# Optimization experiments

Hardware: AMD Instinct MI355X
Metric: run time of the kernel (lower is better)

The kernel has to match this reference:

```python
import jax, jax.numpy as jnp
import numpy as np

MAX_LR = 0.01  # max_learning_rate
NS_A, NS_B, NS_C = 3.4445, -4.7750, 2.0315  # muon Newton-Schulz quintic coefficients


def newtonschulz5(G, steps=5, eps=1e-7):
    # Orthogonalize the last two dims of G (batched over leading dims).
    transpose = G.shape[-2] > G.shape[-1]
    X = jnp.swapaxes(G, -2, -1) if transpose else G
    X = X / (jnp.linalg.norm(X, axis=(-2, -1), keepdims=True) + eps)
    for _ in range(steps):
        A = X @ jnp.swapaxes(X, -2, -1)
        Bm = NS_B * A + NS_C * (A @ A)
        X = NS_A * X + Bm @ X
    return jnp.swapaxes(X, -2, -1) if transpose else X


def setup_inputs() -> dict:
    key = jax.random.key(0)
    ks = jax.random.split(key, 9)
    B, N, D, H, DH = 4, 1024, 1024, 8, 64
    s = D ** -0.5  # scale fast-weight init for numerical sanity (math unchanged)
    return {
        'tokens': jax.random.normal(ks[0], (B, N, D), jnp.float32),
        'wq': jax.random.normal(ks[1], (H, D, DH), jnp.float32) * s,
        'wk': jax.random.normal(ks[2], (H, D, DH), jnp.float32) * s,
        'wv': jax.random.normal(ks[3], (H, D, DH), jnp.float32) * s,
        'wo': jax.random.normal(ks[4], (H, DH, D), jnp.float32) * s,
        'w_lr': jax.random.normal(ks[5], (D, 2), jnp.float32) * 0.02,      # to_learning_rate (no bias)
        'w_target': jax.random.normal(ks[6], (D, D), jnp.float32) * 0.02,  # to_target_values linear (no bias)
        'w_gates': jax.random.normal(ks[7], (D, H), jnp.float32) * 0.02,   # to_gates linear (no bias)
        'rms_w': jnp.ones((D,), jnp.float32),                              # RMSNorm weight
    }


def reference(tokens, wq, wk, wv, wo, w_lr, w_target, w_gates, rms_w):
    N = tokens.shape[1]
    scale = wq.shape[-1] ** -0.5
    eps = jnp.finfo(tokens.dtype).eps

    # RMSNorm
    t = tokens * jax.lax.rsqrt(jnp.mean(tokens * tokens, -1, keepdims=True) + eps) * rms_w

    # gates: b n h -> b h n 1
    gates = jnp.swapaxes(jax.nn.sigmoid(t @ w_gates), -2, -1)[..., None]

    # per-batch fast weights == shared params (past_mem=None), broadcast over b via einsum
    q = jnp.einsum('bnd,hde->bhne', t, wq)
    k = jnp.einsum('bnd,hde->bhne', t, wk)
    v = jnp.einsum('bnd,hde->bhne', t, wv)

    score = jnp.einsum('bhie,bhje->bhij', q, k) * scale
    causal_mask = jnp.triu(jnp.ones((N, N), bool), 1)
    score = jnp.where(causal_mask, -jnp.finfo(score.dtype).max, score)
    attn = jax.nn.softmax(score, axis=-1)
    out = jnp.einsum('bhij,bhje->bhie', attn, v) * gates
    pred_values = jnp.einsum('bhne,hed->bnd', out, wo)

    # target values: linear + LayerNorm (no affine) on shifted tokens
    tv = t[:, 1:] @ w_target
    tv = (tv - tv.mean(-1, keepdims=True)) * jax.lax.rsqrt(tv.var(-1, keepdims=True) + 1e-5)

    # drop last position everywhere
    ts = t[:, :-1]
    pv = pred_values[:, :-1]
    o = out[:, :, :-1]
    g = gates[:, :, :-1]
    a = attn[:, :, :-1, :-1]
    qs, ks_, vs = q[:, :, :-1], k[:, :, :-1], v[:, :, :-1]

    lrs = jax.nn.sigmoid(ts @ w_lr) * MAX_LR  # b (n-1) 2
    lr, mlr = lrs[..., 0], lrs[..., 1]

    # hand-derived backward through the attention fast-weight readout
    error = tv - pv
    dout = jnp.einsum('bnd,hed->bhne', error, wo)
    du = dout * g
    delta = jnp.sum(dout * o, -1, keepdims=True)
    dv = jnp.einsum('bhij,bhie->bhje', a, du)
    dattn = jnp.einsum('bhje,bhie->bhij', vs, du)
    dscore = scale * a * (dattn - delta)
    dq = jnp.einsum('bhje,bhij->bhie', ks_, dscore)
    dk = jnp.einsum('bhie,bhij->bhje', qs, dscore)

    t_qk = ts * lr[..., None]
    t_v = ts * mlr[..., None]
    o_wo = o * mlr[:, None, :, None]

    dwq = jnp.einsum('bhie,bid->bhde', dq, t_qk)
    dwk = jnp.einsum('bhje,bjd->bhde', dk, t_qk)
    dwv = jnp.einsum('bhje,bjd->bhde', dv, t_v)
    dwo = jnp.einsum('bnd,bhne->bhed', error, o_wo)

    dwv = newtonschulz5(dwv)  # muon orthogonalization
    dwo = newtonschulz5(dwo)

    return pred_values, dwq, dwk, dwv, dwo
```

## Files before the change

kernel.cpp:

```cpp
#include <hip/hip_runtime.h>
#include <hip/hip_bf16.h>
#include <math.h>

#define BB 4
#define NN 1024
#define DD 1024
#define HH 8
#define DH 64
#define NSR 1023

#define NS_Ac 3.4445f
#define NS_Bc (-4.775f)
#define NS_Cc 2.0315f

typedef short bf16x8 __attribute__((ext_vector_type(8)));
typedef float f32x4 __attribute__((ext_vector_type(4)));
#define MFMA16(a,b,c) __builtin_amdgcn_mfma_f32_16x16x32_bf16(a,b,c,0,0,0)

#define QS 72
#define TS 40
#define GS 40

static __device__ __forceinline__ float ldin(const void* p, size_t i, int f) {
  return f ? ((const float*)p)[i] : __bfloat162float(((const __hip_bfloat16*)p)[i]);
// ... 74 lines not shown
  const void* src; short* dst; int sld, dld, srow0, scol0, drow0; size_t soff = 0;
  if (bx < 384) {
    int x = bx & 15, y = bx >> 4;
    int n0 = y*64; int which = n0 >> 9, h = (n0 >> 6) & 7;
    src = (which==0) ? wq : (which==1) ? wk : wv;
    soff = (size_t)h*65536;
    sld = 64; dld = 1024; srow0 = x*64; scol0 = 0; drow0 = n0; dst = BqkvT;
  } else if (bx < 640) {
    int r = bx - 384; int x = r & 15, y = r >> 4;
    src = w_target; dst = wtT; sld = 1024; dld = 1024;
    srow0 = x*64; scol0 = y*64; drow0 = scol0;
  } else {
    int r = bx - 640; int x = r & 7, y = r >> 3;
    src = wo; dst = woT2; sld = 1024; dld = 512;
    srow0 = x*64; scol0 = y*64; drow0 = scol0;
  }
  __shared__ float T[64][65];
  int r4 = tid >> 4, c4 = (tid & 15)*4;
  for (int rr = r4; rr < 64; rr += 16)
#pragma unroll
    for (int j = 0; j < 4; j++)
      T[rr][c4+j] = ldin(src, soff + (size_t)(srow0+rr)*sld + scol0 + c4 + j, f);
  __syncthreads();
  int dc = tid >> 2, seg = tid & 3;
  bf16x8 o1, o2;
#pragma unroll
  for (int j = 0; j < 8; j++) { o1[j] = f2bs(T[seg*16+j][dc]); o2[j] = f2bs(T[seg*16+8+j][dc]); }
  *(bf16x8*)&dst[(size_t)(drow0+dc)*dld + srow0 + seg*16]     = o1;
  *(bf16x8*)&dst[(size_t)(drow0+dc)*dld + srow0 + seg*16 + 8] = o2;
}

__global__ __launch_bounds__(256) void k_transp(
    const float* __restrict__ src, size_t sStepZ, int sld,
    short* __restrict__ dst, size_t dStepZ, int dld,
    const float* __restrict__ coef, int zIsBh, int nz)
{
  int z = blockIdx.z;
  const float* sb = src + (size_t)z*sStepZ;
  short* db = dst + (size_t)z*dStepZ;
  const float* cb = coef ? coef + (size_t)(zIsBh ? (z>>3) : z)*1024 : (const float*)0;
  int x0 = blockIdx.x*64, y0 = blockIdx.y*64;
  __shared__ float T[64][65];
  int tid = threadIdx.x;
  int r4 = tid >> 4, c4 = (tid & 15)*4;
  for (int rr = r4; rr < 64; rr += 16) {
    int rg = x0 + rr;
    bool val = rg < nz;
    float cf = val ? (cb ? cb[rg] : 1.f) : 0.f;
    float4 v = val ? *(const float4*)&sb[(size_t)rg*sld + y0 + c4] : make_float4(0,0,0,0);
    T[rr][c4+0] = v.x*cf; T[rr][c4+1] = v.y*cf; T[rr][c4+2] = v.z*cf; T[rr][c4+3] = v.w*cf;
  }
  __syncthreads();
  int dc = tid >> 2, seg = tid & 3;
  bf16x8 o1, o2;
#pragma unroll
  for (int j = 0; j < 8; j++) { o1[j] = f2bs(T[seg*16+j][dc]); o2[j] = f2bs(T[seg*16+8+j][dc]); }
  *(bf16x8*)&db[(size_t)(y0+dc)*dld + x0 + seg*16]     = o1;
  *(bf16x8*)&db[(size_t)(y0+dc)*dld + x0 + seg*16 + 8] = o2;
}

__global__ __launch_bounds__(256) void k_transp5(
    const float* __restrict__ dq, const float* __restrict__ dk, const float* __restrict__ dv,
    const float* __restrict__ predf, const float* __restrict__ o,
    short* __restrict__ dqT, short* __restrict__ dkT, short* __restrict__ dvT,
    short* __restrict__ errT, short* __restrict__ oT,
    const float* __restrict__ lr, const float* __restrict__ mlr)
{
  int bx = blockIdx.x;
  const float* src; short* dst; const float* cb; int sld, dld, x0, y0;
  size_t sStep, dStep; int z;
  if (bx < 1536) {
    int which = bx >> 9; int r = bx & 511;
    z = r >> 4; x0 = (r & 15)*64; y0 = 0;
    sld = 64; dld = 1024; sStep = 65536; dStep = 65536;
    if (which == 0)      { src = dq; dst = dqT; cb = lr; }
    else if (which == 1) { src = dk; dst = dkT; cb = lr; }
    else                 { src = dv; dst = dvT; cb = mlr; }
    cb += (size_t)(z >> 3)*1024;
  } else if (bx < 2560) {
    int r = bx - 1536; z = r >> 8; x0 = (r & 15)*64; y0 = ((r >> 4) & 15)*64;
    src = predf; dst = errT; cb = (const float*)0;
    sld = 1024; dld = 1024; sStep = 1048576; dStep = 1048576;
  } else {
    int r = bx - 2560; z = r >> 7; x0 = (r & 15)*64; y0 = ((r >> 4) & 7)*64;
    src = o; dst = oT; cb = mlr + (size_t)z*1024;
    sld = 512; dld = 1024; sStep = 524288; dStep = 524288;
  }
  src += (size_t)z*sStep; dst += (size_t)z*dStep;
  __shared__ float T[64][65];
  int tid = threadIdx.x;
  int r4 = tid >> 4, c4 = (tid & 15)*4;
  for (int rr = r4; rr < 64; rr += 16) {
    int rg = x0 + rr;
    bool val = rg < 1023;
    float cf = val ? (cb ? cb[rg] : 1.f) : 0.f;
    float4 v = val ? *(const float4*)&src[(size_t)rg*sld + y0 + c4] : make_float4(0,0,0,0);
    T[rr][c4+0] = v.x*cf; T[rr][c4+1] = v.y*cf; T[rr][c4+2] = v.z*cf; T[rr][c4+3] = v.w*cf;
  }
  __syncthreads();
  int dc = tid >> 2, seg = tid & 3;
  bf16x8 o1, o2;
#pragma unroll
  for (int j = 0; j < 8; j++) { o1[j] = f2bs(T[seg*16+j][dc]); o2[j] = f2bs(T[seg*16+8+j][dc]); }
  *(bf16x8*)&dst[(size_t)(y0+dc)*dld + x0 + seg*16]     = o1;
  *(bf16x8*)&dst[(size_t)(y0+dc)*dld + x0 + seg*16 + 8] = o2;
}

__global__ void k_rmsnorm(const void* __restrict__ tokens, const float* __restrict__ rms_f,
                          const float* __restrict__ gw, const float* __restrict__ lrw,
                          float* __restrict__ t, short* __restrict__ t_bf,
                          float* __restrict__ gates, float* __restrict__ lr, float* __restrict__ mlr,
                          const int* __restrict__ flag) {
  const int f = *flag;
  int row = blockIdx.x;
  int b = row >> 10, n = row & 1023;
  __shared__ float red[256];
  __shared__ float red2[4][10];
  float xv[4]; float acc = 0.f;
#pragma unroll
  for (int i = 0; i < 4; i++) {
    xv[i] = ldin(tokens, (size_t)row*DD + threadIdx.x + 256*i, f);
    acc += xv[i]*xv[i];
  }
  red[threadIdx.x] = acc; __syncthreads();
  for (int s = 128; s > 0; s >>= 1) { if (threadIdx.x < s) red[threadIdx.x] += red[threadIdx.x+s]; __syncthreads(); }
  float r = rsqrtf(red[0] / DD + 1.1920929e-07f);
  float a10[10] = {0,0,0,0,0,0,0,0,0,0};
#pragma unroll
  for (int i = 0; i < 4; i++) {
    int d = threadIdx.x + 256*i;
    float v = xv[i] * r * rms_f[d];
    t[(size_t)row*DD + d] = v;
    t_bf[(size_t)row*DD + d] = f2bs(v);
#pragma unroll
    for (int h = 0; h < HH; h++) a10[h] += v * gw[d*HH + h];
    a10[8] += v * lrw[d*2];
    a10[9] += v * lrw[d*2+1];
  }
  int lane = threadIdx.x & 63, w = threadIdx.x >> 6;
#pragma unroll
  for (int c = 0; c < 10; c++) {
    float a = a10[c];
    for (int s = 32; s > 0; s >>= 1) a += __shfl_xor(a, s, 64);
    if (lane == 0) red2[w][c] = a;
  }
  __syncthreads();
  if (threadIdx.x < 10) {
    int c = threadIdx.x;
    float sum = red2[0][c]+red2[1][c]+red2[2][c]+red2[3][c];
    float sg = 1.f / (1.f + __expf(-sum));
    if (c < 8)      gates[((size_t)b*HH + c)*NN + n] = sg;
    else if (c == 8) lr[row]  = sg * 0.01f;
    else             mlr[row] = sg * 0.01f;
  }
}

__global__ __launch_bounds__(256) void k_gemm_bf(
    const short* __restrict__ A, const short* __restrict__ B,
    int lda, int ldb, int K, int M, int rowmode, int ep,
    size_t aStepBh, size_t aStepB, size_t bStepBh, size_t bStepB,
    float* __restrict__ O0, short* __restrict__ OS, void* __restrict__ OD,
    size_t out_off, const float* __restrict__ gates, const int* __restrict__ flag,
    const short* __restrict__ A2, const short* __restrict__ B2,
    size_t bStepB2, size_t out_off2, int ldb2)
{
  int z = blockIdx.z;
  const short* Au = A; const short* Bu = B;
  size_t bStepBv = bStepB; size_t out_offv = out_off;
  int epv = ep; int ldbv = ldb;
  if (ep == 4 && z >= 32) { Bu = B2; out_offv = out_off2; z -= 32; }
  if (ep == 5 && z >= 32) { Au = A2; Bu = B2; bStepBv = bStepB2; ldbv = ldb2; epv = 6; z -= 32; }
  int zb = z >> 3;
  const short* Ab = Au + (size_t)z*aStepBh + (size_t)zb*aStepB;
  const short* Bb = Bu + (size_t)z*bStepBh + (size_t)zb*bStepBv;
  int m0 = blockIdx.x*64, n0 = blockIdx.y*64;
  __shared__ __align__(16) short AsBs[5120];
  short* As = AsBs;
  short* Bs = AsBs + 2560;
  int tid = threadIdx.x;
  int lane = tid & 63, w = tid >> 6;
  int l15 = lane & 15, quad = lane >> 4;
  int row = tid >> 2, col8 = (tid & 3)*8;
  int r = m0 + row;
  int arow;
  if (rowmode == 1)      { int b = r / 1023; arow = r + b + 1; }
  else if (rowmode == 2) { int b = r / 1023; arow = r + b; }
  else arow = r;
  bool aval = (r < M);
  const short* Ap = Ab + (size_t)arow*lda + col8;
  const short* Bp = Bb + (size_t)(n0+row)*ldbv + col8;
  f32x4 acc[4] = {fz4(),fz4(),fz4(),fz4()};
  bf16x8 av = aval ? *(const bf16x8*)(Ap) : bz8();
  bf16x8 bv = *(const bf16x8*)(Bp);
  for (int kb = 0; kb < K; kb += 32) {
    __syncthreads();
    *(bf16x8*)&As[row*GS + col8] = av;
    *(bf16x8*)&Bs[row*GS + col8] = bv;
    __syncthreads();
    if (kb + 32 < K) {
      av = aval ? *(const bf16x8*)(Ap + kb + 32) : bz8();
      bv = *(const bf16x8*)(Bp + kb + 32);
    }
    bf16x8 afr = *(const bf16x8*)&As[(w*16 + l15)*GS + quad*8];
#pragma unroll
    for (int es = 0; es < 4; es++) {
      bf16x8 bfr = *(const bf16x8*)&Bs[(es*16 + l15)*GS + quad*8];
      acc[es] = MFMA16(afr, bfr, acc[es]);
    }
  }
  const int f = flag ? *flag : 1;
#pragma unroll
  for (int es = 0; es < 4; es++) {
#pragma unroll
    for (int rix = 0; rix < 4; rix++) {
      int rr = m0 + w*16 + quad*4 + rix;
      if (rr >= M) continue;
      int c = n0 + es*16 + l15;
      float val = acc[es][rix];
      if (epv == 0) {
        int which = c >> 9; int h = (c >> 6) & 7; int e = c & 63;
        int b = rr >> 10; int n = rr & 1023;
        OS[(size_t)which*2097152 + (((size_t)b*8 + h)*1024 + n)*64 + e] = f2bs(val);
      } else if (epv == 1) {
        O0[(size_t)rr*1024 + c] = val;
        stout(OD, (size_t)rr*1024 + c, val, f);
      } else if (epv == 2) {
        O0[(size_t)rr*1024 + c] = val;
      } else if (epv == 3) {
        int b = rr / 1023; int n = rr % 1023;
        int h = c >> 6;
        float g = gates[((size_t)b*8 + h)*1024 + n];
        OS[((size_t)b*1024 + n)*512 + c] = f2bs(val * g);
      } else if (epv == 4) {
        stout(OD, out_offv + ((size_t)z*1024 + rr)*64 + c, val, f);
      } else if (epv == 5) {
        O0[((size_t)z*64 + rr)*1024 + c] = val;
      } else {
        O0[((size_t)(32 + z)*64 + rr)*1024 + c] = val;
      }
    }
  }
  if (epv == 0 && (n0 >> 9) == 2) {
    short* vt = (short*)OD;
    int h = (n0 >> 6) & 7;
    int bb = m0 >> 10;
    int bh = bb*8 + h;
    int nloc = m0 & 1023;
    __syncthreads();
#pragma unroll
    for (int es = 0; es < 4; es++)
#pragma unroll
      for (int rix = 0; rix < 4; rix++)
        AsBs[(es*16 + l15)*72 + (w*16 + quad*4 + rix)] = f2bs(acc[es][rix]);
    __syncthreads();
    int e = tid >> 2, nseg = (tid & 3)*16;
    bf16x8 v1 = *(const bf16x8*)&AsBs[e*72 + nseg];
    bf16x8 v2 = *(const bf16x8*)&AsBs[e*72 + nseg + 8];
    size_t dsti = ((size_t)bh*64 + e)*1024 + nloc + nseg;
    *(bf16x8*)&vt[dsti]     = v1;
    *(bf16x8*)&vt[dsti + 8] = v2;
  }
}

__global__ __launch_bounds__(256) void k_attn_fwd(
    const short* __restrict__ qb, const short* __restrict__ kb, const short* __restrict__ vbT,
    const float* __restrict__ gates,
    float* __restrict__ o, short* __restrict__ o_bf,
    float* __restrict__ mrow, float* __restrict__ lrow)
{
  int pp = blockIdx.x >> 8;
  int xx = (blockIdx.x >> 5) & 7;
  int bh = blockIdx.x & 31;
  int it = pp ? xx : (15 - xx);
  int i0 = it*64;
  int b = bh >> 3, h = bh & 7;
  __shared__ __align__(16) short Qs[64*QS];
  __shared__ __align__(16) short Ks[32*QS];
  __shared__ __align__(16) short VsT[64*TS];
  __shared__ __align__(16) short Ps[64*TS];
  int tid = threadIdx.x;
  int lane = tid & 63, w = tid >> 6;
  int l15 = lane & 15, quad = lane >> 4;
  int sr = tid >> 3, sc = (tid & 7) * 8;
  int sr2 = tid >> 2, sc2 = (tid & 3) * 8;
  int rsw = (l15 >> 2) & 3;
  for (int rr = sr; rr < 64; rr += 32)
    *(bf16x8*)&Qs[rr*QS + sc] = *(const bf16x8*)&qb[((size_t)bh*1024 + i0 + rr)*64 + sc];
  f32x4 oa[4] = {fz4(),fz4(),fz4(),fz4()};
  float m_st[4] = {-1e30f,-1e30f,-1e30f,-1e30f};
  float l_st[4] = {0.f,0.f,0.f,0.f};
  int jiters = 2*it + 2;
  bf16x8 rk = *(const bf16x8*)&kb[((size_t)bh*1024 + sr)*64 + sc];
  bf16x8 rv = *(const bf16x8*)&vbT[((size_t)bh*64 + sr2)*1024 + sc2];
  for (int jc = 0; jc < jiters; jc++) {
    int j0 = jc*32;
    __syncthreads();
    *(bf16x8*)&Ks[sr*QS + sc]    = rk;
    *(bf16x8*)&VsT[sr2*TS + sc2] = rv;
    __syncthreads();
    if (jc + 1 < jiters) {
      int j1 = j0 + 32;
      rk = *(const bf16x8*)&kb[((size_t)bh*1024 + j1 + sr)*64 + sc];
      rv = *(const bf16x8*)&vbT[((size_t)bh*64 + sr2)*1024 + j1 + sc2];
    }
    f32x4 sa[2] = {fz4(),fz4()};
#pragma unroll
    for (int kc = 0; kc < 64; kc += 32) {
      bf16x8 afr = *(const bf16x8*)&Qs[(w*16 + l15)*QS + kc + quad*8];
#pragma unroll
      for (int ni = 0; ni < 2; ni++) {
        bf16x8 bfr = *(const bf16x8*)&Ks[(ni*16 + l15)*QS + kc + quad*8];
        sa[ni] = MFMA16(afr, bfr, sa[ni]);
      }
    }
#pragma unroll
    for (int r = 0; r < 4; r++) {
      int gi = i0 + w*16 + quad*4 + r;
      float s0 = sa[0][r]*0.125f, s1 = sa[1][r]*0.125f;
      if (j0 + l15 > gi)      s0 = -1e30f;
      if (j0 + 16 + l15 > gi) s1 = -1e30f;
      float rm = fmaxf(s0, s1);
      rm = fmaxf(rm, __shfl_xor(rm, 1, 64));
      rm = fmaxf(rm, __shfl_xor(rm, 2, 64));
      rm = fmaxf(rm, __shfl_xor(rm, 4, 64));
      rm = fmaxf(rm, __shfl_xor(rm, 8, 64));
      float m_new = fmaxf(m_st[r], rm);
      float alpha = __expf(m_st[r] - m_new);
      float p0 = __expf(s0 - m_new), p1 = __expf(s1 - m_new);
      float rs = p0 + p1;
      rs += __shfl_xor(rs, 1, 64);
      rs += __shfl_xor(rs, 2, 64);
      rs += __shfl_xor(rs, 4, 64);
      rs += __shfl_xor(rs, 8, 64);
      l_st[r] = l_st[r]*alpha + rs;
      m_st[r] = m_new;
#pragma unroll
      for (int es = 0; es < 4; es++) oa[es][r] *= alpha;
      int rowp = w*16 + quad*4 + r;
      int lo3 = l15 & 7, g0 = l15 >> 3;
      Ps[rowp*TS + ((( g0      ^ quad) << 3) | lo3)] = f2bs(p0);
      Ps[rowp*TS + ((((g0 | 2) ^ quad) << 3) | lo3)] = f2bs(p1);
    }
    bf16x8 pa = *(const bf16x8*)&Ps[(w*16 + l15)*TS + ((quad ^ rsw) << 3)];
#pragma unroll
    for (int es = 0; es < 4; es++) {
      bf16x8 bv = *(const bf16x8*)&VsT[(es*16 + l15)*TS + quad*8];
      oa[es] = MFMA16(pa, bv, oa[es]);
    }
  }
#pragma unroll
  for (int r = 0; r < 4; r++) {
    int gi = i0 + w*16 + quad*4 + r;
    float g = gates[(size_t)bh*1024 + gi] / l_st[r];
#pragma unroll
    for (int es = 0; es < 4; es++) {
      float val = oa[es][r] * g;
      size_t oi = ((size_t)b*1024 + gi)*512 + h*64 + es*16 + l15;
      o[oi] = val;
      o_bf[oi] = f2bs(val);
    }
    if (l15 == 0) {
      mrow[(size_t)bh*1024 + gi] = m_st[r];
      lrow[(size_t)bh*1024 + gi] = l_st[r];
    }
  }
}

__global__ void k_lnsub(const float* __restrict__ tvbuf, float* __restrict__ predf,
                        short* __restrict__ err_bf) {
  int r = blockIdx.x; int b = r / 1023; int prow = r + b;
  const float* tvr = tvbuf + (size_t)r*1024;
  __shared__ float red[256];
  float s1 = 0.f, s2 = 0.f;
  float xv[4];
#pragma unroll
  for (int i = 0; i < 4; i++) {
    xv[i] = tvr[threadIdx.x + 256*i];
    s1 += xv[i]; s2 += xv[i]*xv[i];
  }
  red[threadIdx.x] = s1; __syncthreads();
  for (int s = 128; s > 0; s >>= 1){ if (threadIdx.x < s) red[threadIdx.x] += red[threadIdx.x+s]; __syncthreads(); }
  float mean = red[0] / 1024.f; __syncthreads();
  red[threadIdx.x] = s2; __syncthreads();
  for (int s = 128; s > 0; s >>= 1){ if (threadIdx.x < s) red[threadIdx.x] += red[threadIdx.x+s]; __syncthreads(); }
  float var = red[0]/1024.f - mean*mean;
  float rstd = rsqrtf(var + 1e-5f);
  float* er = predf + (size_t)prow*1024;
#pragma unroll
  for (int i = 0; i < 4; i++) {
    int d = threadIdx.x + 256*i;
    float e = (xv[i]-mean)*rstd - er[d];
    er[d] = e;
    err_bf[(size_t)prow*1024 + d] = f2bs(e);
  }
}

__global__ __launch_bounds__(256) void k_t16(const short* __restrict__ qv, const short* __restrict__ du,
                                             short* __restrict__ kbT, short* __restrict__ duT,
                                             short* __restrict__ qbT,
                                             const float* __restrict__ o, const float* __restrict__ gates,
                                             float* __restrict__ delta) {
  int bx = blockIdx.x; int tid = threadIdx.x;
  if (bx >= 1536) {
    int r = bx - 1536; int b = r / 1023; int n = r % 1023;
    int w = tid >> 6, lane = tid & 63;
    size_t base = ((size_t)b*1024 + n)*512;
    float p1 = bs2f(du[base + tid])       * o[base + tid];
    float p2 = bs2f(du[base + tid + 256]) * o[base + tid + 256];
    for (int s = 32; s > 0; s >>= 1) { p1 += __shfl_xor(p1, s, 64); p2 += __shfl_xor(p2, s, 64); }
    if (lane == 0) {
      size_t i1 = ((size_t)b*8 + w)*1024 + n;
      size_t i2 = ((size_t)b*8 + w + 4)*1024 + n;
      delta[i1] = p1 / gates[i1];
// ... 102 lines not shown
        rdu  = (g1 < NSR) ? *(const bf16x8*)&du_bf[((size_t)b*1024 + g1)*512 + h*64 + sc] : bz8();
        rqT  = *(const bf16x8*)&qbT[((size_t)bh*64 + sr2)*1024 + i1 + sc2];
        rduT = *(const bf16x8*)&duT[((size_t)bh*64 + sr2)*1024 + i1 + sc2];
        if (tid < 32) {
          int gi2 = i1 + tid;
          rm = mrow[(size_t)bh*1024 + gi2];
          rl = lrow[(size_t)bh*1024 + gi2];
          rd = (gi2 < NSR) ? delta[(size_t)bh*1024 + gi2] : 0.f;
        }
      }
      f32x4 st[2] = {fz4(),fz4()};
      f32x4 dt[2] = {fz4(),fz4()};
#pragma unroll
      for (int kc = 0; kc < 64; kc += 32) {
        bf16x8 ak = *(const bf16x8*)&Ks[(w*16 + l15)*QS + kc + quad*8];
        bf16x8 av = *(const bf16x8*)&Vs[(w*16 + l15)*QS + kc + quad*8];
#pragma unroll
        for (int ni = 0; ni < 2; ni++) {
          bf16x8 bq = *(const bf16x8*)&Qs[(ni*16 + l15)*QS + kc + quad*8];
          bf16x8 bd = *(const bf16x8*)&DUs[(ni*16 + l15)*QS + kc + quad*8];
          st[ni] = MFMA16(ak, bq, st[ni]);
          dt[ni] = MFMA16(av, bd, dt[ni]);
        }
      }
#pragma unroll
      for (int ni = 0; ni < 2; ni++)
#pragma unroll
        for (int r = 0; r < 4; r++) {
          int gj = j0 + w*16 + quad*4 + r;
          int il = ni*16 + l15;
          int gi = i0c + il;
          float p = 0.f, dsc = 0.f;
          if (gi >= gj && gi < NSR && gj < NSR) {
            p = __expf(st[ni][r]*0.125f - mvs[il]) * lvs[il];
            dsc = 0.125f*p*(dt[ni][r] - dls[il]);
          }
          int rowp = w*16 + quad*4 + r;
          int pc = ((((ni << 1) | (l15 >> 3)) ^ quad) << 3) | (l15 & 7);
          PsT[rowp*TS + pc] = f2bs(p);
          DsT[rowp*TS + pc] = f2bs(dsc);
        }
      int rc = (quad ^ rsw) << 3;
      bf16x8 ap = *(const bf16x8*)&PsT[(w*16 + l15)*TS + rc];
      bf16x8 ad = *(const bf16x8*)&DsT[(w*16 + l15)*TS + rc];
#pragma unroll
      for (int es = 0; es < 4; es++) {
        bf16x8 bdu = *(const bf16x8*)&DUsT[(es*16 + l15)*TS + quad*8];
        bf16x8 bqt = *(const bf16x8*)&QsT[(es*16 + l15)*TS + quad*8];
        dva[es] = MFMA16(ap, bdu, dva[es]);
        dka[es] = MFMA16(ad, bqt, dka[es]);
      }
    }
#pragma unroll
    for (int r = 0; r < 4; r++) {
      int gj = j0 + w*16 + quad*4 + r;
#pragma unroll
      for (int es = 0; es < 4; es++) {
        dv[((size_t)bh*1024 + gj)*64 + es*16 + l15] = dva[es][r];
        dk[((size_t)bh*1024 + gj)*64 + es*16 + l15] = dka[es][r];
      }
    }
  } else {
    int bid = blockIdx.x - 512;
    int pp = bid >> 8;
    int xx = (bid >> 5) & 7;
    int bh = bid & 31;
    int it = pp ? xx : (15 - xx);
    int i0 = it*64;
    int b = bh >> 3, h = bh & 7;
    short* Qs  = smem;
    short* DUs = Qs + 4608;
    short* Ks  = DUs + 4608;
    short* Vs  = Ks + 2304;
    short* KsT = Vs + 2304;
    short* DsN = KsT + 2560;
    for (int rr = sr; rr < 64; rr += 32) {
      int gi = i0 + rr;
      *(bf16x8*)&Qs[rr*QS + sc] = *(const bf16x8*)&qb[((size_t)bh*1024 + gi)*64 + sc];
      bf16x8 duv = (gi < NSR) ? *(const bf16x8*)&du_bf[((size_t)b*1024 + gi)*512 + h*64 + sc] : bz8();
      *(bf16x8*)&DUs[rr*QS + sc] = duv;
    }
    float m4[4], li4[4], dl4[4];
#pragma unroll
    for (int r = 0; r < 4; r++) {
      int gi = i0 + w*16 + quad*4 + r;
      m4[r]  = mrow[(size_t)bh*1024 + gi];
      li4[r] = 1.f / lrow[(size_t)bh*1024 + gi];
      dl4[r] = (gi < NSR) ? delta[(size_t)bh*1024 + gi] : 0.f;
    }
    f32x4 dqa[4] = {fz4(),fz4(),fz4(),fz4()};
    int jiters = 2*it + 2;
    bf16x8 rk  = *(const bf16x8*)&kb[((size_t)bh*1024 + sr)*64 + sc];
    bf16x8 rv  = *(const bf16x8*)&vb[((size_t)bh*1024 + sr)*64 + sc];
    bf16x8 rkT = *(const bf16x8*)&kbT[((size_t)bh*64 + sr2)*1024 + sc2];
    for (int jc = 0; jc < jiters; jc++) {
      int j0 = jc*32;
      __syncthreads();
      *(bf16x8*)&Ks[sr*QS + sc]    = rk;
      *(bf16x8*)&Vs[sr*QS + sc]    = rv;
      *(bf16x8*)&KsT[sr2*TS + sc2] = rkT;
      __syncthreads();
      if (jc + 1 < jiters) {
        int j1 = j0 + 32;
        rk  = *(const bf16x8*)&kb[((size_t)bh*1024 + j1 + sr)*64 + sc];
        rv  = *(const bf16x8*)&vb[((size_t)bh*1024 + j1 + sr)*64 + sc];
        rkT = *(const bf16x8*)&kbT[((size_t)bh*64 + sr2)*1024 + j1 + sc2];
      }
      f32x4 st[2] = {fz4(),fz4()};
      f32x4 dt[2] = {fz4(),fz4()};
#pragma unroll
      for (int kc = 0; kc < 64; kc += 32) {
        bf16x8 aq = *(const bf16x8*)&Qs[(w*16 + l15)*QS + kc + quad*8];
        bf16x8 adu = *(const bf16x8*)&DUs[(w*16 + l15)*QS + kc + quad*8];
#pragma unroll
        for (int ni = 0; ni < 2; ni++) {
          bf16x8 bk = *(const bf16x8*)&Ks[(ni*16 + l15)*QS + kc + quad*8];
          bf16x8 bv = *(const bf16x8*)&Vs[(ni*16 + l15)*QS + kc + quad*8];
          st[ni] = MFMA16(aq, bk, st[ni]);
          dt[ni] = MFMA16(adu, bv, dt[ni]);
        }
      }
#pragma unroll
      for (int ni = 0; ni < 2; ni++)
#pragma unroll
        for (int r = 0; r < 4; r++) {
          int gi = i0 + w*16 + quad*4 + r;
          int gj = j0 + ni*16 + l15;
          float dsc = 0.f;
          if (gi >= gj && gi < NSR && gj < NSR) {
            float p = __expf(st[ni][r]*0.125f - m4[r]) * li4[r];
            dsc = 0.125f*p*(dt[ni][r] - dl4[r]);
          }
          int rowp = w*16 + quad*4 + r;
          int pc = ((((ni << 1) | (l15 >> 3)) ^ quad) << 3) | (l15 & 7);
          DsN[rowp*TS + pc] = f2bs(dsc);
        }
      bf16x8 ads = *(const bf16x8*)&DsN[(w*16 + l15)*TS + ((quad ^ rsw) << 3)];
#pragma unroll
      for (int es = 0; es < 4; es++) {
        bf16x8 bkt = *(const bf16x8*)&KsT[(es*16 + l15)*TS + quad*8];
        dqa[es] = MFMA16(ads, bkt, dqa[es]);
      }
    }
#pragma unroll
    for (int r = 0; r < 4; r++) {
      int gi = i0 + w*16 + quad*4 + r;
#pragma unroll
      for (int es = 0; es < 4; es++)
        dq[((size_t)bh*1024 + gi)*64 + es*16 + l15] = dqa[es][r];
    }
  }
}

__global__ __launch_bounds__(256) void k_ns_all(const float* __restrict__ Xsrc, float* __restrict__ Ydst) {
  int m = blockIdx.x;
  const float* Xm = Xsrc + (size_t)m*DH*DD;
  float* Ym = Ydst + (size_t)m*DH*DD;
  __shared__ __align__(16) short nsm[46080];
  __shared__ float redz[4];
  short* Mhi  = nsm;
  short* Mlo  = nsm + 4608;
  short* MThi = nsm + 2*4608;
  short* MTlo = nsm + 3*4608;
  short* A0hi = nsm + 4*4608;
  short* A0lo = nsm + 5*4608;
  short* Shi  = nsm + 6*4608;
  short* Slo  = nsm + 7*4608;
  short* Aihi = nsm + 8*4608;
  short* Ailo = nsm + 9*4608;
  short* XGhi = Shi;
  short* XGlo = Slo;
  short* XThi = Aihi;
  short* XTlo = Ailo;
  int tid = threadIdx.x;
  int lane = tid & 63, w = tid >> 6;
  int l15 = lane & 15, quad = lane >> 4;
  int srow = tid >> 2, scol = (tid & 3) * 8;
  f32x4 accA[4] = {fz4(),fz4(),fz4(),fz4()};
  float ss = 0.f;
  float4 c1 = *(const float4*)&Xm[(size_t)srow*1024 + scol];
  float4 c2 = *(const float4*)&Xm[(size_t)srow*1024 + scol + 4];
  for (int kb = 0; kb < 1024; kb += 32) {
    float xv[8] = {c1.x,c1.y,c1.z,c1.w,c2.x,c2.y,c2.z,c2.w};
    bf16x8 hi, lo;
#pragma unroll
    for (int j = 0; j < 8; j++) {
      short h = f2bs(xv[j]);
      hi[j] = h; lo[j] = f2bs(xv[j] - bs2f(h));
      ss += xv[j]*xv[j];
    }
    __syncthreads();
    *(bf16x8*)&XGhi[srow*GS + scol] = hi;
    *(bf16x8*)&XGlo[srow*GS + scol] = lo;
    __syncthreads();
    if (kb + 32 < 1024) {
      c1 = *(const float4*)&Xm[(size_t)srow*1024 + kb + 32 + scol];
      c2 = *(const float4*)&Xm[(size_t)srow*1024 + kb + 32 + scol + 4];
    }
    bf16x8 ah = *(const bf16x8*)&XGhi[(w*16 + l15)*GS + quad*8];
    bf16x8 al = *(const bf16x8*)&XGlo[(w*16 + l15)*GS + quad*8];
#pragma unroll
    for (int es = 0; es < 4; es++) {
      bf16x8 bh = *(const bf16x8*)&XGhi[(es*16 + l15)*GS + quad*8];
      bf16x8 bl = *(const bf16x8*)&XGlo[(es*16 + l15)*GS + quad*8];
      accA[es] = MFMA16(ah, bh, accA[es]);
      accA[es] = MFMA16(ah, bl, accA[es]);
      accA[es] = MFMA16(al, bh, accA[es]);
    }
  }
  for (int s = 32; s > 0; s >>= 1) ss += __shfl_xor(ss, s, 64);
  __syncthreads();
  if (lane == 0) redz[w] = ss;
  __syncthreads();
  float tot = redz[0]+redz[1]+redz[2]+redz[3];
  float r_ = 1.f / (sqrtf(tot) + 1e-7f);
  float r2 = r_ * r_;
  __syncthreads();
#pragma unroll
  for (int es = 0; es < 4; es++)
#pragma unroll
    for (int rr = 0; rr < 4; rr++) {
      int row = w*16 + quad*4 + rr, col = es*16 + l15;
      float v = accA[es][rr] * r2;
      short h = f2bs(v);
      A0hi[row*QS + col] = h;
      A0lo[row*QS + col] = f2bs(v - bs2f(h));
      short ih = (row == col) ? (short)0x3F80 : (short)0;
      Mhi[row*QS + col] = ih;  Mlo[row*QS + col] = 0;
      MThi[row*QS + col] = ih; MTlo[row*QS + col] = 0;
    }
  __syncthreads();
  for (int itn = 0; itn < 5; itn++) {
    f32x4 s4[4] = {fz4(),fz4(),fz4(),fz4()};
    mm64(Mhi, Mlo, A0hi, A0lo, s4, w, l15, quad);
    st_hl(Shi, Slo, s4, w, l15, quad);
    __syncthreads();
    f32x4 ai4[4] = {fz4(),fz4(),fz4(),fz4()};
    mm64(Shi, Slo, Mhi, Mlo, ai4, w, l15, quad);
    st_hl(Aihi, Ailo, ai4, w, l15, quad);
    __syncthreads();
    f32x4 a24[4] = {fz4(),fz4(),fz4(),fz4()};
    mm64(Aihi, Ailo, Aihi, Ailo, a24, w, l15, quad);
    f32x4 b4[4];
#pragma unroll
    for (int es = 0; es < 4; es++) b4[es] = NS_Bc*ai4[es] + NS_Cc*a24[es];
    st_hl(Shi, Slo, b4, w, l15, quad);
    __syncthreads();
    f32x4 m4[4] = {fz4(),fz4(),fz4(),fz4()};
    mm64(Shi, Slo, MThi, MTlo, m4, w, l15, quad);
#pragma unroll
    for (int es = 0; es < 4; es++)
#pragma unroll
      for (int rr = 0; rr < 4; rr++) {
        int row = w*16 + quad*4 + rr, col = es*16 + l15;
        float mold = bs2f(Mhi[row*QS + col]) + bs2f(Mlo[row*QS + col]);
        m4[es][rr] = NS_Ac*mold + m4[es][rr];
      }
    __syncthreads();
#pragma unroll
    for (int es = 0; es < 4; es++)
#pragma unroll
      for (int rr = 0; rr < 4; rr++) {
        int row = w*16 + quad*4 + rr, col = es*16 + l15;
        float x = m4[es][rr];
        short h = f2bs(x);
        short lo = f2bs(x - bs2f(h));
        Mhi[row*QS + col] = h;  Mlo[row*QS + col] = lo;
        MThi[col*QS + row] = h; MTlo[col*QS + row] = lo;
      }
    __syncthreads();
  }
  float4 d1 = *(const float4*)&Xm[(size_t)srow*1024 + scol];
  float4 d2 = *(const float4*)&Xm[(size_t)srow*1024 + scol + 4];
  float4 d3 = *(const float4*)&Xm[(size_t)srow*1024 + scol + 32];
  float4 d4 = *(const float4*)&Xm[(size_t)srow*1024 + scol + 36];
  for (int c0 = 0; c0 < 1024; c0 += 64) {
    __syncthreads();
    {
      float xv0[8] = {d1.x,d1.y,d1.z,d1.w,d2.x,d2.y,d2.z,d2.w};
      float xv1[8] = {d3.x,d3.y,d3.z,d3.w,d4.x,d4.y,d4.z,d4.w};
#pragma unroll
      for (int j = 0; j < 8; j++) {
        int n0 = scol + j;
        short h0 = f2bs(xv0[j]);
        XThi[n0*QS + srow] = h0;
        XTlo[n0*QS + srow] = f2bs(xv0[j] - bs2f(h0));
        int n1 = scol + 32 + j;
        short h1 = f2bs(xv1[j]);
        XThi[n1*QS + srow] = h1;
        XTlo[n1*QS + srow] = f2bs(xv1[j] - bs2f(h1));
      }
    }
    __syncthreads();
    if (c0 + 64 < 1024) {
      d1 = *(const float4*)&Xm[(size_t)srow*1024 + c0 + 64 + scol];
      d2 = *(const float4*)&Xm[(size_t)srow*1024 + c0 + 64 + scol + 4];
      d3 = *(const float4*)&Xm[(size_t)srow*1024 + c0 + 64 + scol + 32];
      d4 = *(const float4*)&Xm[(size_t)srow*1024 + c0 + 64 + scol + 36];
    }
    f32x4 u4[4] = {fz4(),fz4(),fz4(),fz4()};
    mm64(Mhi, Mlo, XThi, XTlo, u4, w, l15, quad);
#pragma unroll
    for (int es = 0; es < 4; es++)
#pragma unroll
      for (int rr = 0; rr < 4; rr++) {
        int row = w*16 + quad*4 + rr, col = c0 + es*16 + l15;
        Ym[(size_t)row*1024 + col] = r_ * u4[es][rr];
      }
  }
}

__global__ void k_ns_out(const float* __restrict__ X, void* __restrict__ d_outv,
                         size_t off_dwv, size_t off_dwo, const int* __restrict__ flag) {
  const int f = *flag;
  int idx = blockIdx.x*256 + threadIdx.x;
  int e = idx % DH; int d = (idx / DH) % DD; int bh = idx / (DH*DD);
  stout(d_outv, off_dwv + idx, X[((size_t)bh*DH + e)*DD + d], f);
  stout(d_outv, off_dwo + idx, X[(size_t)32*DH*DD + idx], f);
}

extern "C" void kernel_launch(void* const* d_in, const int* in_sizes, int n_in,
                              void* d_out, int out_size, void* d_ws, size_t ws_size,
                              hipStream_t stream) {
  const void* tokens   = d_in[0];
  const void* wq       = d_in[1];
  const void* wk       = d_in[2];
  const void* wv       = d_in[3];
  const void* wo       = d_in[4];
  const void* w_lr     = d_in[5];
  const void* w_target = d_in[6];
  const void* w_gates  = d_in[7];
  const void* rms_w    = d_in[8];

  const size_t off_dwq  = 4194304;
  const size_t off_dwk  = 6291456;
  const size_t off_dwv  = 8388608;
  const size_t off_dwo  = 10485760;

  float* ws = (float*)d_ws;
  float* t_    = ws;
  float* tvbuf = ws;
  short* errT  = (short*)ws;
  short* oT    = (short*)(ws + 2097152);
  short* t_bf  = (short*)(ws + 4194304);
  short* err_bf= (short*)(ws + 4194304);
  short* tT    = (short*)(ws + 6291456);
  short* qb    = (short*)(ws + 8388608);
  short* kbuf  = qb + 2097152;
  short* vbuf  = qb + 4194304;
  short* dqT   = (short*)(ws + 8388608);
  short* dkT   = dqT + 2097152;
  short* dvT   = dqT + 4194304;
  float* o_    = ws + 11534336;
  short* o_bf  = (short*)(ws + 13631488);
  short* du_bf = (short*)(ws + 13631488);
  float* predf = ws + 14680064;
  float* Xns   = ws + 14680064;
  short* BqkvT = (short*)(ws + 18874368);
  short* wtT   = (short*)(ws + 19660800);
  short* woT2  = (short*)(ws + 20185088);
  short* wo_bf = (short*)(ws + 20447232);
  float* gw    = ws + 20709376;
  float* lrw   = ws + 20717568;
  float* rms_f = ws + 20719616;
  float* dv_   = ws + 18874368;
  float* dk_   = ws + 20971520;
  float* dq_   = ws + 23068672;
  float* Yns   = ws + 18874368;
  float* gates_= ws + 25165824;
  float* mrow_ = ws + 25198592;
  float* lrow_ = ws + 25231360;
  float* delta_= ws + 25264128;
  float* lr_   = ws + 25296896;
  float* mlr_  = ws + 25300992;
  int*   flag_ = (int*)(ws + 25305088);
  short* vbT = (short*)(ws + 3145728);
  short* duT = (short*)(ws + 3145728);
  short* kbT = (short*)(ws + 4194304);
  short* qbT = (short*)ws;

  hipLaunchKernelGGL(k_prep, dim3(1324), dim3(256), 0, stream, wq, wk, wv, w_target, wo, w_lr, w_gates, rms_w,
                     BqkvT, wtT, woT2, wo_bf, lrw, gw, rms_f, flag_);
  hipLaunchKernelGGL(k_rmsnorm, dim3(BB*NN), dim3(256), 0, stream, tokens, rms_f, gw, lrw,
                     t_, t_bf, gates_, lr_, mlr_, flag_);
  hipLaunchKernelGGL(k_transp, dim3(64,16,1), dim3(256), 0, stream, t_, (size_t)0, 1024, tT, (size_t)0, 4096, (const float*)nullptr, 0, 4096);

  hipLaunchKernelGGL(k_gemm_bf, dim3(64,24,1), dim3(256), 0, stream, t_bf, BqkvT, 1024, 1024, 1024, 4096, 0, 0,
                     (size_t)0,(size_t)0,(size_t)0,(size_t)0, (float*)nullptr, qb, (void*)vbT, (size_t)0,
                     (const float*)nullptr, flag_, (const short*)nullptr, (const short*)nullptr, (size_t)0, (size_t)0, 0);
  hipLaunchKernelGGL(k_attn_fwd, dim3(512), dim3(256), 0, stream, qb, kbuf, vbT, gates_, o_, o_bf, mrow_, lrow_);
  hipLaunchKernelGGL(k_gemm_bf, dim3(64,16,1), dim3(256), 0, stream, o_bf, woT2, 512, 512, 512, 4096, 0, 1,
                     (size_t)0,(size_t)0,(size_t)0,(size_t)0, predf, (short*)nullptr, d_out, (size_t)0,
                     (const float*)nullptr, flag_, (const short*)nullptr, (const short*)nullptr, (size_t)0, (size_t)0, 0);
  hipLaunchKernelGGL(k_gemm_bf, dim3(64,16,1), dim3(256), 0, stream, t_bf, wtT, 1024, 1024, 1024, 4092, 1, 2,
                     (size_t)0,(size_t)0,(size_t)0,(size_t)0, tvbuf, (short*)nullptr, (void*)nullptr, (size_t)0,
                     (const float*)nullptr, flag_, (const short*)nullptr, (const short*)nullptr, (size_t)0, (size_t)0, 0);
  hipLaunchKernelGGL(k_lnsub, dim3(BB*NSR), dim3(256), 0, stream, tvbuf, predf, err_bf);
  hipLaunchKernelGGL(k_gemm_bf, dim3(64,8,1), dim3(256), 0, stream, err_bf, wo_bf, 1024, 1024, 1024, 4092, 2, 3,
                     (size_t)0,(size_t)0,(size_t)0,(size_t)0, (float*)nullptr, du_bf, (void*)nullptr, (size_t)0,
                     gates_, flag_, (const short*)nullptr, (const short*)nullptr, (size_t)0, (size_t)0, 0);
  hipLaunchKernelGGL(k_t16, dim3(1536 + BB*NSR), dim3(256), 0, stream, (const short*)qb, (const short*)du_bf,
                     kbT, duT, qbT, o_, gates_, delta_);
  hipLaunchKernelGGL(k_bwd, dim3(1024), dim3(256), 0, stream, qb, kbuf, vbuf, du_bf, qbT, duT, kbT,
                     mrow_, lrow_, delta_, dv_, dk_, dq_);
  hipLaunchKernelGGL(k_transp5, dim3(3072), dim3(256), 0, stream, dq_, dk_, dv_, predf, o_,
                     dqT, dkT, dvT, errT, oT, lr_, mlr_);
  hipLaunchKernelGGL(k_gemm_bf, dim3(16,1,64), dim3(256), 0, stream, tT, dqT, 4096, 1024, 1024, 1024, 0, 4,
                     (size_t)0,(size_t)1024,(size_t)65536,(size_t)0, (float*)nullptr, (short*)nullptr, d_out, off_dwq,
                     (const float*)nullptr, flag_, (const short*)nullptr, (const short*)dkT, (size_t)0, off_dwk, 1024);
  hipLaunchKernelGGL(k_gemm_bf, dim3(1,16,64), dim3(256), 0, stream, dvT, tT, 1024, 4096, 1024, 64, 0, 5,
                     (size_t)65536,(size_t)0,(size_t)0,(size_t)1024, Xns, (short*)nullptr, (void*)nullptr, (size_t)0,
                     (const float*)nullptr, flag_, (const short*)oT, (const short*)errT, (size_t)1048576, (size_t)0, 1024);
  hipLaunchKernelGGL(k_ns_all, dim3(64), dim3(256), 0, stream, Xns, Yns);
  hipLaunchKernelGGL(k_ns_out, dim3(8192), dim3(256), 0, stream, Yns, d_out, off_dwv, off_dwo, flag_);
  (void)in_sizes; (void)n_in; (void)out_size; (void)ws_size;
}
```

Baseline: 469.1 us.

## Add 128x128 register-blocked GEMM kernel and fuse Newton-Schulz output store

Adds a new GEMM kernel that tiles 128x128 outputs per block, with each wave computing a 4x4 set of MFMA tiles. It is used for the QKV projection, the output projection, the target projection and the error backprojection, including the V-transpose epilogue. This gives more operand reuse per LDS load than the old 64-wide tile. The Newton-Schulz kernel now writes dwv (transposed through LDS) and dwo straight to the output, which drops the separate k_ns_out pass and its intermediate buffer. Larger tiles mean fewer blocks and more registers per thread, which may hurt occupancy on the smaller GEMMs.

New measurement: 503.1 us. 7.3% more time.

```diff
diff --git a/kernel.cpp b/kernel.cpp
--- a/kernel.cpp
+++ b/kernel.cpp
@@ -250,6 +250,121 @@
     if (c < 8)      gates[((size_t)b*HH + c)*NN + n] = sg;
     else if (c == 8) lr[row]  = sg * 0.01f;
     else             mlr[row] = sg * 0.01f;
+  }
+}
+
+__global__ __launch_bounds__(256) void k_gemm2(
+    const short* __restrict__ A, const short* __restrict__ B,
+    int lda, int ldb, int K, int M, int rowmode, int ep,
+    float* __restrict__ O0, short* __restrict__ OS, void* __restrict__ OD,
+    short* __restrict__ VT, const float* __restrict__ gates, const int* __restrict__ flag)
+{
+  int m0 = blockIdx.x*128, n0 = blockIdx.y*128;
+  __shared__ __align__(16) short sm2[17408];
+  short* As = sm2;
+  short* Bs = sm2 + 5120;
+  int tid = threadIdx.x;
+  int lane = tid & 63, w = tid >> 6;
+  int wr = w >> 1, wc = w & 1;
+  int l15 = lane & 15, quad = lane >> 4;
+  int row = tid >> 1, col16 = (tid & 1)*16;
+  int r = m0 + row;
+  int arow;
+  if (rowmode == 1)      { int b = r / 1023; arow = r + b + 1; }
+  else if (rowmode == 2) { int b = r / 1023; arow = r + b; }
+  else arow = r;
+  bool aval = (r < M);
+  const short* Ap = A + (size_t)arow*lda + col16;
+  const short* Bp = B + (size_t)(n0+row)*ldb + col16;
+  f32x4 acc[4][4];
+#pragma unroll
+  for (int mi = 0; mi < 4; mi++)
+#pragma unroll
+    for (int ni = 0; ni < 4; ni++) acc[mi][ni] = fz4();
+  bf16x8 av0 = aval ? *(const bf16x8*)(Ap) : bz8();
+  bf16x8 av1 = aval ? *(const bf16x8*)(Ap + 8) : bz8();
+  bf16x8 bv0 = *(const bf16x8*)(Bp);
+  bf16x8 bv1 = *(const bf16x8*)(Bp + 8);
+  for (int kb = 0; kb < K; kb += 32) {
+    __syncthreads();
+    *(bf16x8*)&As[row*GS + col16]     = av0;
+    *(bf16x8*)&As[row*GS + col16 + 8] = av1;
+    *(bf16x8*)&Bs[row*GS + col16]     = bv0;
+    *(bf16x8*)&Bs[row*GS + col16 + 8] = bv1;
+    __syncthreads();
+    if (kb + 32 < K) {
+      av0 = aval ? *(const bf16x8*)(Ap + kb + 32) : bz8();
+      av1 = aval ? *(const bf16x8*)(Ap + kb + 40) : bz8();
+      bv0 = *(const bf16x8*)(Bp + kb + 32);
+      bv1 = *(const bf16x8*)(Bp + kb + 40);
+    }
+    bf16x8 afr[4], bfr[4];
+#pragma unroll
+    for (int mi = 0; mi < 4; mi++)
+      afr[mi] = *(const bf16x8*)&As[(wr*64 + mi*16 + l15)*GS + quad*8];
+#pragma unroll
+    for (int ni = 0; ni < 4; ni++)
+      bfr[ni] = *(const bf16x8*)&Bs[(wc*64 + ni*16 + l15)*GS + quad*8];
+#pragma unroll
+    for (int mi = 0; mi < 4; mi++)
+#pragma unroll
+      for (int ni = 0; ni < 4; ni++)
+        acc[mi][ni] = MFMA16(afr[mi], bfr[ni], acc[mi][ni]);
+  }
+  const int f = flag ? *flag : 1;
+#pragma unroll
+  for (int mi = 0; mi < 4; mi++)
+#pragma unroll
+    for (int ni = 0; ni < 4; ni++)
+#pragma unroll
+      for (int rix = 0; rix < 4; rix++) {
+        int rr = m0 + wr*64 + mi*16 + quad*4 + rix;
+        if (rr >= M) continue;
+        int c = n0 + wc*64 + ni*16 + l15;
+        float val = acc[mi][ni][rix];
+        if (ep == 0) {
+          int which = c >> 9; int h = (c >> 6) & 7; int e = c & 63;
+          int b = rr >> 10; int n = rr & 1023;
+          OS[(size_t)which*2097152 + (((size_t)b*8 + h)*1024 + n)*64 + e] = f2bs(val);
+        } else if (ep == 1) {
+          O0[(size_t)rr*1024 + c] = val;
+          stout(OD, (size_t)rr*1024 + c, val, f);
+        } else if (ep == 2) {
+          O0[(size_t)rr*1024 + c] = val;
+        } else {
+          int b = rr / 1023; int n = rr % 1023;
+          int h = c >> 6;
+          float g = gates[((size_t)b*8 + h)*1024 + n];
+          OS[((size_t)b*1024 + n)*512 + c] = f2bs(val * g);
+        }
+      }
+  if (ep == 0 && n0 >= 1024) {
+    short* ST = sm2;
+    __syncthreads();
+#pragma unroll
+    for (int mi = 0; mi < 4; mi++)
+#pragma unroll
+      for (int ni = 0; ni < 4; ni++)
+#pragma unroll
+        for (int rix = 0; rix < 4; rix++) {
+          int ml = wr*64 + mi*16 + quad*4 + rix;
+          int cl = wc*64 + ni*16 + l15;
+          int mo = ml + ((ml >> 6) << 3);
+          ST[cl*136 + mo] = f2bs(acc[mi][ni][rix]);
+        }
+    __syncthreads();
+    int r2 = tid >> 1;
+    int sg = tid & 1;
+    int cg = n0 + r2;
+    int h = (cg >> 6) & 7;
+    int e = cg & 63;
+    int b = m0 >> 10;
+    int bh = b*8 + h;
+    size_t dst = ((size_t)bh*64 + e)*1024 + (m0 & 1023) + sg*64;
+    int so = r2*136 + sg*72;
+#pragma unroll
+    for (int j = 0; j < 64; j += 8)
+      *(bf16x8*)&VT[dst + j] = *(const bf16x8*)&ST[so + j];
   }
 }
 
@@ -315,48 +430,14 @@
       if (rr >= M) continue;
       int c = n0 + es*16 + l15;
       float val = acc[es][rix];
-      if (epv == 0) {
-        int which = c >> 9; int h = (c >> 6) & 7; int e = c & 63;
-        int b = rr >> 10; int n = rr & 1023;
-        OS[(size_t)which*2097152 + (((size_t)b*8 + h)*1024 + n)*64 + e] = f2bs(val);
-      } else if (epv == 1) {
-        O0[(size_t)rr*1024 + c] = val;
-        stout(OD, (size_t)rr*1024 + c, val, f);
-      } else if (epv == 2) {
-        O0[(size_t)rr*1024 + c] = val;
-      } else if (epv == 3) {
-        int b = rr / 1023; int n = rr % 1023;
-        int h = c >> 6;
-        float g = gates[((size_t)b*8 + h)*1024 + n];
-        OS[((size_t)b*1024 + n)*512 + c] = f2bs(val * g);
-      } else if (epv == 4) {
+      if (epv == 4) {
         stout(OD, out_offv + ((size_t)z*1024 + rr)*64 + c, val, f);
       } else if (epv == 5) {
         O0[((size_t)z*64 + rr)*1024 + c] = val;
-      } else {
+      } else if (epv == 6) {
         O0[((size_t)(32 + z)*64 + rr)*1024 + c] = val;
       }
     }
-  }
-  if (epv == 0 && (n0 >> 9) == 2) {
-    short* vt = (short*)OD;
-    int h = (n0 >> 6) & 7;
-    int bb = m0 >> 10;
-    int bh = bb*8 + h;
-    int nloc = m0 & 1023;
-    __syncthreads();
-#pragma unroll
-    for (int es = 0; es < 4; es++)
-#pragma unroll
-      for (int rix = 0; rix < 4; rix++)
-        AsBs[(es*16 + l15)*72 + (w*16 + quad*4 + rix)] = f2bs(acc[es][rix]);
-    __syncthreads();
-    int e = tid >> 2, nseg = (tid & 3)*16;
-    bf16x8 v1 = *(const bf16x8*)&AsBs[e*72 + nseg];
-    bf16x8 v2 = *(const bf16x8*)&AsBs[e*72 + nseg + 8];
-    size_t dsti = ((size_t)bh*64 + e)*1024 + nloc + nseg;
-    *(bf16x8*)&vt[dsti]     = v1;
-    *(bf16x8*)&vt[dsti + 8] = v2;
   }
 }
 
@@ -765,10 +846,11 @@
   }
 }
 
-__global__ __launch_bounds__(256) void k_ns_all(const float* __restrict__ Xsrc, float* __restrict__ Ydst) {
+__global__ __launch_bounds__(256) void k_ns_all(const float* __restrict__ Xsrc, void* __restrict__ d_outv,
+                                                size_t off_dwv, size_t off_dwo, const int* __restrict__ flag) {
   int m = blockIdx.x;
   const float* Xm = Xsrc + (size_t)m*DH*DD;
-  float* Ym = Ydst + (size_t)m*DH*DD;
+  const int f = *flag;
   __shared__ __align__(16) short nsm[46080];
   __shared__ float redz[4];
   short* Mhi  = nsm;
@@ -883,6 +965,7 @@
       }
     __syncthreads();
   }
+  float* Sf = (float*)Shi;
   float4 d1 = *(const float4*)&Xm[(size_t)srow*1024 + scol];
   float4 d2 = *(const float4*)&Xm[(size_t)srow*1024 + scol + 4];
   float4 d3 = *(const float4*)&Xm[(size_t)srow*1024 + scol + 32];
@@ -913,23 +996,30 @@
     }
     f32x4 u4[4] = {fz4(),fz4(),fz4(),fz4()};
     mm64(Mhi, Mlo, XThi, XTlo, u4, w, l15, quad);
-#pragma unroll
-    for (int es = 0; es < 4; es++)
-#pragma unroll
-      for (int rr = 0; rr < 4; rr++) {
-        int row = w*16 + quad*4 + rr, col = c0 + es*16 + l15;
-        Ym[(size_t)row*1024 + col] = r_ * u4[es][rr];
-      }
-  }
-}
-
-__global__ void k_ns_out(const float* __restrict__ X, void* __restrict__ d_outv,
-                         size_t off_dwv, size_t off_dwo, const int* __restrict__ flag) {
-  const int f = *flag;
-  int idx = blockIdx.x*256 + threadIdx.x;
-  int e = idx % DH; int d = (idx / DH) % DD; int bh = idx / (DH*DD);
-  stout(d_outv, off_dwv + idx, X[((size_t)bh*DH + e)*DD + d], f);
-  stout(d_outv, off_dwo + idx, X[(size_t)32*DH*DD + idx], f);
+    if (m >= 32) {
+#pragma unroll
+      for (int es = 0; es < 4; es++)
+#pragma unroll
+        for (int rr = 0; rr < 4; rr++) {
+          int row = w*16 + quad*4 + rr, col = c0 + es*16 + l15;
+          stout(d_outv, off_dwo + (size_t)(m-32)*65536 + (size_t)row*1024 + col, r_*u4[es][rr], f);
+        }
+    } else {
+#pragma unroll
+      for (int es = 0; es < 4; es++)
+#pragma unroll
+        for (int rr = 0; rr < 4; rr++) {
+          int row = w*16 + quad*4 + rr, col = es*16 + l15;
+          Sf[col*65 + row] = r_*u4[es][rr];
+        }
+      __syncthreads();
+      int dl = tid >> 2, e0 = (tid & 3)*16;
+      size_t ob = off_dwv + (size_t)m*65536 + (size_t)(c0 + dl)*64 + e0;
+#pragma unroll
+      for (int j = 0; j < 16; j++)
+        stout(d_outv, ob + j, Sf[dl*65 + e0 + j], f);
+    }
+  }
 }
 
 extern "C" void kernel_launch(void* const* d_in, const int* in_sizes, int n_in,
@@ -979,7 +1069,6 @@
   float* dv_   = ws + 18874368;
   float* dk_   = ws + 20971520;
   float* dq_   = ws + 23068672;
-  float* Yns   = ws + 18874368;
   float* gates_= ws + 25165824;
   float* mrow_ = ws + 25198592;
   float* lrow_ = ws + 25231360;
@@ -998,20 +1087,16 @@
                      t_, t_bf, gates_, lr_, mlr_, flag_);
   hipLaunchKernelGGL(k_transp, dim3(64,16,1), dim3(256), 0, stream, t_, (size_t)0, 1024, tT, (size_t)0, 4096, (const float*)nullptr, 0, 4096);
 
-  hipLaunchKernelGGL(k_gemm_bf, dim3(64,24,1), dim3(256), 0, stream, t_bf, BqkvT, 1024, 1024, 1024, 4096, 0, 0,
-                     (size_t)0,(size_t)0,(size_t)0,(size_t)0, (float*)nullptr, qb, (void*)vbT, (size_t)0,
-                     (const float*)nullptr, flag_, (const short*)nullptr, (const short*)nullptr, (size_t)0, (size_t)0, 0);
+  hipLaunchKernelGGL(k_gemm2, dim3(32,12), dim3(256), 0, stream, t_bf, BqkvT, 1024, 1024, 1024, 4096, 0, 0,
+                     (float*)nullptr, qb, (void*)nullptr, vbT, (const float*)nullptr, flag_);
   hipLaunchKernelGGL(k_attn_fwd, dim3(512), dim3(256), 0, stream, qb, kbuf, vbT, gates_, o_, o_bf, mrow_, lrow_);
-  hipLaunchKernelGGL(k_gemm_bf, dim3(64,16,1), dim3(256), 0, stream, o_bf, woT2, 512, 512, 512, 4096, 0, 1,
-                     (size_t)0,(size_t)0,(size_t)0,(size_t)0, predf, (short*)nullptr, d_out, (size_t)0,
-                     (const float*)nullptr, flag_, (const short*)nullptr, (const short*)nullptr, (size_t)0, (size_t)0, 0);
-  hipLaunchKernelGGL(k_gemm_bf, dim3(64,16,1), dim3(256), 0, stream, t_bf, wtT, 1024, 1024, 1024, 4092, 1, 2,
-                     (size_t)0,(size_t)0,(size_t)0,(size_t)0, tvbuf, (short*)nullptr, (void*)nullptr, (size_t)0,
-                     (const float*)nullptr, flag_, (const short*)nullptr, (const short*)nullptr, (size_t)0, (size_t)0, 0);
+  hipLaunchKernelGGL(k_gemm2, dim3(32,8), dim3(256), 0, stream, o_bf, woT2, 512, 512, 512, 4096, 0, 1,
+                     predf, (short*)nullptr, d_out, (short*)nullptr, (const float*)nullptr, flag_);
+  hipLaunchKernelGGL(k_gemm2, dim3(32,8), dim3(256), 0, stream, t_bf, wtT, 1024, 1024, 1024, 4092, 1, 2,
+                     tvbuf, (short*)nullptr, (void*)nullptr, (short*)nullptr, (const float*)nullptr, flag_);
   hipLaunchKernelGGL(k_lnsub, dim3(BB*NSR), dim3(256), 0, stream, tvbuf, predf, err_bf);
-  hipLaunchKernelGGL(k_gemm_bf, dim3(64,8,1), dim3(256), 0, stream, err_bf, wo_bf, 1024, 1024, 1024, 4092, 2, 3,
-                     (size_t)0,(size_t)0,(size_t)0,(size_t)0, (float*)nullptr, du_bf, (void*)nullptr, (size_t)0,
-                     gates_, flag_, (const short*)nullptr, (const short*)nullptr, (size_t)0, (size_t)0, 0);
+  hipLaunchKernelGGL(k_gemm2, dim3(32,4), dim3(256), 0, stream, err_bf, wo_bf, 1024, 1024, 1024, 4092, 2, 3,
+                     (float*)nullptr, du_bf, (void*)nullptr, (short*)nullptr, gates_, flag_);
   hipLaunchKernelGGL(k_t16, dim3(1536 + BB*NSR), dim3(256), 0, stream, (const short*)qb, (const short*)du_bf,
                      kbT, duT, qbT, o_, gates_, delta_);
   hipLaunchKernelGGL(k_bwd, dim3(1024), dim3(256), 0, stream, qb, kbuf, vbuf, du_bf, qbT, duT, kbT,
@@ -1024,7 +1109,6 @@
   hipLaunchKernelGGL(k_gemm_bf, dim3(1,16,64), dim3(256), 0, stream, dvT, tT, 1024, 4096, 1024, 64, 0, 5,
                      (size_t)65536,(size_t)0,(size_t)0,(size_t)1024, Xns, (short*)nullptr, (void*)nullptr, (size_t)0,
                      (const float*)nullptr, flag_, (const short*)oT, (const short*)errT, (size_t)1048576, (size_t)0, 1024);
-  hipLaunchKernelGGL(k_ns_all, dim3(64), dim3(256), 0, stream, Xns, Yns);
-  hipLaunchKernelGGL(k_ns_out, dim3(8192), dim3(256), 0, stream, Yns, d_out, off_dwv, off_dwo, flag_);
+  hipLaunchKernelGGL(k_ns_all, dim3(64), dim3(256), 0, stream, Xns, d_out, off_dwv, off_dwo, flag_);
   (void)in_sizes; (void)n_in; (void)out_size; (void)ws_size;
 }
```
